# Kernel optimization log

Measured on AMD Instinct MI355X. Metric: run time of the kernel, lower is better.

The kernel has to match this reference:

```python
import jax, jax.numpy as jnp
import numpy as np
from jax import lax

H, MEM, AUX = 1024, 256, 16
S = MEM + AUX          # total_slots
B, T = 8, 4096
TOPK = 8               # top_k_binding
GAMMA, BETA, PTS = 0.92, 0.08, 0.4  # gamma, beta, prediction_torque_scale
RANK = 10              # coupling_rank == prediction_rank


def _inv_softplus(v):
    return float(np.log(np.expm1(max(float(v), 1e-6))))


def setup_inputs() -> dict:
    key = jax.random.key(0)
    ks = jax.random.split(key, 8)
    x = jax.random.normal(ks[0], (B, T, H), dtype=jnp.float32)
    # base basis: orthonormal columns in the first MEM slots (memory_dim < hidden_dim -> QR branch)
    q, _ = jnp.linalg.qr(jax.random.normal(ks[1], (H, MEM), dtype=jnp.float32))
    basis = jnp.zeros((H, S), jnp.float32).at[:, :MEM].set(q)
    return dict(
        x=x,
        basis=basis,
        tape_init_re=jax.random.normal(ks[2], (S,), dtype=jnp.float32) / S ** 0.5,
        tape_init_im=jax.random.normal(ks[3], (S,), dtype=jnp.float32) / S ** 0.5,
        eta_raw=jnp.asarray(_inv_softplus(0.08), jnp.float32),
        alpha=jnp.asarray(0.35, jnp.float32),
        torque_rotation=jnp.zeros((S,), jnp.float32),
        w_r=jnp.zeros((S,), jnp.float32),
        breadth_gate=jnp.zeros((S,), jnp.float32),
        epsilon_factor=jax.random.normal(ks[4], (S, RANK), dtype=jnp.float32) * 0.02,
        epsilon_scale=jnp.zeros((RANK,), jnp.float32),
        epsilon_diag=jnp.zeros((S,), jnp.float32),
        pred_factor=jax.random.normal(ks[5], (S, RANK), dtype=jnp.float32) * 0.02,
        pred_scale=jnp.zeros((RANK,), jnp.float32),
        pred_diag=jnp.zeros((S,), jnp.float32),
    )


def _forward(x, basis, tape_init_re, tape_init_im, eta_raw, alpha,
             torque_rotation, w_r, breadth_gate,
             epsilon_factor, epsilon_scale, epsilon_diag,
             pred_factor, pred_scale, pred_diag):
    active = jnp.arange(S) < MEM                      # base slots active (fixed population)
    amf = active.astype(jnp.float32)
    eta = jax.nn.softplus(eta_raw)
    # low-rank Hermitian coupling epsilon and prediction operator W_pred
    eps = (epsilon_factor * epsilon_scale) @ epsilon_factor.T + jnp.diag(epsilon_diag)
    wp = (pred_factor * pred_scale) @ pred_factor.T + jnp.diag(pred_diag)
    eps_c = eps.astype(jnp.complex64)
    wp_c = wp.astype(jnp.complex64)
    rot = jnp.exp(1j * torque_rotation.astype(jnp.complex64))  # torque phase rotation
    wr_gate = jax.nn.sigmoid(w_r)
    bg = jax.nn.sigmoid(breadth_gate)

    def renorm(tape):
        masked = tape * amf
        nrm = jnp.sqrt(jnp.maximum((jnp.abs(masked) ** 2).sum(-1, keepdims=True), 1e-16))
        return masked / nrm

    tape0 = (tape_init_re + 1j * tape_init_im) * amf   # aux slots zeroed as in _complex_tape_init
    tape0 = renorm(jnp.broadcast_to(tape0, (B, S)))

    def step(carry, x_t):
        tape, prev = carry                              # [B,S] complex64 each
        m = jnp.einsum('hs,bh->bs', basis, x_t)         # project into slot space
        mag = jnp.abs(m) * amf
        kth = lax.top_k(mag, TOPK)[0][:, -1:]           # top-k binding threshold
        inj = jnp.where((mag >= kth) & active, m, 0.0).astype(jnp.complex64)
        rotated = tape * rot
        drive = jnp.einsum('st,bt->bs', eps_c, rotated)  # coupling drive
        pred = jnp.einsum('st,bt->bs', wp_c, rotated)    # prediction torque
        new = (GAMMA * rotated + eta * drive + BETA * inj
               + PTS * 1j * pred + wr_gate * prev)
        new = renorm(new)
        y = x_t + alpha * jnp.einsum('hs,bs->bh', basis, bg * new.real)
        return (new, tape), y

    (_, _), ys = lax.scan(step, (tape0, tape0), jnp.swapaxes(x, 0, 1))
    return jnp.swapaxes(ys, 0, 1)


def reference(x, basis, tape_init_re, tape_init_im, eta_raw, alpha,
              torque_rotation, w_r, breadth_gate,
              epsilon_factor, epsilon_scale, epsilon_diag,
              pred_factor, pred_scale, pred_diag):
    return _forward(x, basis, tape_init_re, tape_init_im, eta_raw, alpha,
                    torque_rotation, w_r, breadth_gate,
                    epsilon_factor, epsilon_scale, epsilon_diag,
                    pred_factor, pred_scale, pred_diag)
```

## Files before the change

### kernel.cpp

```cpp
#include <hip/hip_runtime.h>
#include <cstdint>
#include <cstddef>

#define HD    1024
#define SLOTS 272
#define MEMS  256
#define BATCH 8
#define TT    4096
#define RR    (BATCH*TT)
#define RANKC 10

#define GAMMA 0.92f
#define BETA  0.08f
#define PTS   0.4f

typedef float f32x2 __attribute__((ext_vector_type(2)));
#define PKFMA(a, b, c) __builtin_elementwise_fma((a), (b), (c))

#define DPP_ADD(v, ctrl, rmask)                                                   \
    v += __int_as_float(__builtin_amdgcn_update_dpp(                              \
        0, __float_as_int(v), (ctrl), (rmask), 0xf, true))

__device__ __forceinline__ float wave_sum_bcast(float v)
{
    DPP_ADD(v, 0xB1,  0xf);
    DPP_ADD(v, 0x4E,  0xf);
    DPP_ADD(v, 0x141, 0xf);
    DPP_ADD(v, 0x140, 0xf);
    DPP_ADD(v, 0x142, 0xa);
    DPP_ADD(v, 0x143, 0xc);
    return __int_as_float(__builtin_amdgcn_readlane(__float_as_int(v), 63));
}

__global__ void prep_kernel(const float* __restrict__ t0re, const float* __restrict__ t0im,
                            const float* __restrict__ eta_raw,
                            const float* __restrict__ trot, const float* __restrict__ w_r,
                            const float* __restrict__ bgate,
                            const float* __restrict__ eps_scale, const float* __restrict__ pred_scale,
                            const float* __restrict__ eps_diag, const float* __restrict__ pred_diag,
                            float* __restrict__ consts, int* __restrict__ flags)
{
    __shared__ float red[MEMS];
    const int s = threadIdx.x;
    const float tr = t0re[s], ti = t0im[s];
    red[s] = tr * tr + ti * ti;
    __syncthreads();
    for (int off = 128; off > 0; off >>= 1) {
        if (s < off) red[s] += red[s + off];
        __syncthreads();
    }
    const float nrm = sqrtf(fmaxf(red[0], 1e-16f));
    const float eta = log1pf(expf(eta_raw[0]));
    const float rc = cosf(trot[s]), rs = sinf(trot[s]);
    const float c1 = GAMMA + eta * eps_diag[s];
    const float c2 = PTS * pred_diag[s];
    consts[0 * MEMS + s] = 1.0f / (1.0f + expf(-w_r[s]));
    consts[1 * MEMS + s] = 1.0f / (1.0f + expf(-bgate[s]));
    consts[2 * MEMS + s] = c1 * rc - c2 * rs;
    consts[3 * MEMS + s] = c1 * rs + c2 * rc;
    consts[4 * MEMS + s] = tr / nrm;
    consts[5 * MEMS + s] = ti / nrm;
    consts[6 * MEMS + s] = rc;
    consts[7 * MEMS + s] = rs;
    if (s == 0) {
        consts[8 * MEMS] = eta;
        int f1 = 0, f2 = 0;
        for (int k = 0; k < RANKC; ++k) {
            if (eps_scale[k]  != 0.0f) f1 = 1;
            if (pred_scale[k] != 0.0f) f2 = 1;
        }
        flags[0] = f1;
        flags[1] = f2;
    }
}

__global__ __launch_bounds__(256) void proj_topk_kernel(const float* __restrict__ x,
                                                        const float* __restrict__ basis,
                                                        float* __restrict__ M)
{
    __shared__ float pAs[16][64];
    __shared__ float pBs[16][260];
    const int tid  = threadIdx.x;
    const size_t row0 = (size_t)blockIdx.x * 64;
    const int mt = tid >> 5;
    const int nt = tid & 31;
    const int ar = tid >> 2;
    const int ak = (tid & 3) * 4;
    const int bk = tid >> 4;
    const int bn = (tid & 15) * 16;
    float acc[2][2][4][4] = {};
    for (int k0 = 0; k0 < HD; k0 += 16) {
        {
            const float4 av = *(const float4*)&x[(row0 + ar) * HD + k0 + ak];
            pAs[ak + 0][ar] = av.x; pAs[ak + 1][ar] = av.y;
            pAs[ak + 2][ar] = av.z; pAs[ak + 3][ar] = av.w;
#pragma unroll
            for (int c = 0; c < 4; ++c) {
                const float4 bv = *(const float4*)&basis[(size_t)(k0 + bk) * SLOTS + bn + c * 4];
                *(float4*)&pBs[bk][bn + c * 4] = bv;
            }
        }
        __syncthreads();
#pragma unroll
        for (int kk = 0; kk < 16; ++kk) {
            const float4 a0 = *(const float4*)&pAs[kk][mt * 4];
            const float4 a1 = *(const float4*)&pAs[kk][32 + mt * 4];
            const float4 b0 = *(const float4*)&pBs[kk][nt * 4];
            const float4 b1 = *(const float4*)&pBs[kk][128 + nt * 4];
            const float av[2][4] = {{a0.x, a0.y, a0.z, a0.w}, {a1.x, a1.y, a1.z, a1.w}};
            const float bv[2][4] = {{b0.x, b0.y, b0.z, b0.w}, {b1.x, b1.y, b1.z, b1.w}};
#pragma unroll
            for (int p = 0; p < 2; ++p)
#pragma unroll
                for (int q = 0; q < 2; ++q)
#pragma unroll
                    for (int i = 0; i < 4; ++i)
#pragma unroll
                        for (int j = 0; j < 4; ++j)
                            acc[p][q][i][j] += av[p][i] * bv[q][j];
        }
        __syncthreads();
    }
#pragma unroll
    for (int p = 0; p < 2; ++p)
#pragma unroll
        for (int i = 0; i < 4; ++i) {
            float v[8], a[8], w8[8];
#pragma unroll
            for (int q = 0; q < 2; ++q)
#pragma unroll
                for (int j = 0; j < 4; ++j) {
                    v[q * 4 + j] = acc[p][q][i][j];
                    a[q * 4 + j] = fabsf(v[q * 4 + j]);
                    w8[q * 4 + j] = a[q * 4 + j];
                }
            float kv = 0.0f;
#pragma unroll
            for (int it = 0; it < 8; ++it) {
                float lm = w8[0]; int li = 0;
#pragma unroll
                for (int e = 1; e < 8; ++e)
                    if (w8[e] > lm) { lm = w8[e]; li = e; }
                float bm = lm; int bi = nt * 8 + li;
#pragma unroll
                for (int off = 1; off < 32; off <<= 1) {
                    float om = __shfl_xor(bm, off);
                    int   oi = __shfl_xor(bi, off);
                    if (om > bm || (om == bm && oi < bi)) { bm = om; bi = oi; }
                }
                kv = bm;
                if ((bi >> 3) == nt) w8[bi & 7] = -1.0f;
            }
            const int r = p * 32 + mt * 4 + i;
#pragma unroll
            for (int q = 0; q < 2; ++q) {
                float4 o;
                o.x = (a[q * 4 + 0] >= kv) ? BETA * v[q * 4 + 0] : 0.0f;
                o.y = (a[q * 4 + 1] >= kv) ? BETA * v[q * 4 + 1] : 0.0f;
                o.z = (a[q * 4 + 2] >= kv) ? BETA * v[q * 4 + 2] : 0.0f;
                o.w = (a[q * 4 + 3] >= kv) ? BETA * v[q * 4 + 3] : 0.0f;
                *(float4*)&M[(row0 + r) * MEMS + q * 128 + nt * 4] = o;
            }
        }
}

__global__ __launch_bounds__(64) void scan_kernel(const float* __restrict__ M,
                                                  const float* __restrict__ consts,
                                                  const int* __restrict__ flags,
                                                  const float* __restrict__ eps_fac,
                                                  const float* __restrict__ eps_scale,
                                                  const float* __restrict__ eps_diag,
                                                  const float* __restrict__ pred_fac,
                                                  const float* __restrict__ pred_scale,
                                                  const float* __restrict__ pred_diag,
                                                  float* __restrict__ Wout)
{
    const int b    = blockIdx.x;
    const int lane = threadIdx.x;
    const int s0   = lane * 4;
    const int general = flags[0] | flags[1];
    const size_t base = (size_t)b * TT * MEMS + s0;

    if (!general) {
        f32x2 wrg[2], A2[2], B2[2];
        f32x2 wre[2], wim[2], qre[2], qim[2];
        {
            const float4 w4 = *(const float4*)&consts[0 * MEMS + s0];
            const float4 a4 = *(const float4*)&consts[2 * MEMS + s0];
            const float4 b4 = *(const float4*)&consts[3 * MEMS + s0];
            const float4 r4 = *(const float4*)&consts[4 * MEMS + s0];
            const float4 i4 = *(const float4*)&consts[5 * MEMS + s0];
            wrg[0] = {w4.x, w4.y};  wrg[1] = {w4.z, w4.w};
            A2[0]  = {a4.x, a4.y};  A2[1]  = {a4.z, a4.w};
            B2[0]  = {b4.x, b4.y};  B2[1]  = {b4.z, b4.w};
            wre[0] = {r4.x, r4.y};  wre[1] = {r4.z, r4.w};
            wim[0] = {i4.x, i4.y};  wim[1] = {i4.z, i4.w};
            qre[0] = wre[0]; qre[1] = wre[1];
            qim[0] = wim[0]; qim[1] = wim[1];
        }
        float ssp;
        {
            const f32x2 p0 = PKFMA(wim[0], wim[0], wre[0] * wre[0]);
            const f32x2 p1 = PKFMA(wim[1], wim[1], wre[1] * wre[1]);
            const f32x2 pp = p0 + p1;
            ssp = pp.x + pp.y;
        }
        float4 mbuf[16];
#pragma unroll
        for (int j = 0; j < 16; ++j)
            mbuf[j] = *(const float4*)&M[base + (size_t)j * MEMS];
        for (int t0 = 0; t0 < TT; t0 += 16) {
#pragma unroll
            for (int j = 0; j < 16; ++j) {
                const int t = t0 + j;
                const float4 mc = mbuf[j];
                mbuf[j] = *(const float4*)&M[base + (size_t)(t + 16) * MEMS];
                const float stot = wave_sum_bcast(ssp);
                const float icv  = __builtin_amdgcn_rsqf(fmaxf(stot, 1e-16f));
                const f32x2 ic2  = {icv, icv};
                const f32x2 Lr0 = PKFMA(A2[0], wre[0], -(B2[0] * wim[0]));
                const f32x2 Li0 = PKFMA(B2[0], wre[0],  A2[0] * wim[0]);
                const f32x2 Lr1 = PKFMA(A2[1], wre[1], -(B2[1] * wim[1]));
                const f32x2 Li1 = PKFMA(B2[1], wre[1],  A2[1] * wim[1]);
                const f32x2 m0 = {mc.x, mc.y};
                const f32x2 m1 = {mc.z, mc.w};
                const f32x2 Wr0 = PKFMA(wrg[0], qre[0], m0);
                const f32x2 Wi0 = wrg[0] * qim[0];
                const f32x2 Wr1 = PKFMA(wrg[1], qre[1], m1);
                const f32x2 Wi1 = wrg[1] * qim[1];
                const f32x2 u1r0 = PKFMA(ic2, Lr0, Wr0);
                const f32x2 u1i0 = PKFMA(ic2, Li0, Wi0);
                const f32x2 u1r1 = PKFMA(ic2, Lr1, Wr1);
                const f32x2 u1i1 = PKFMA(ic2, Li1, Wi1);
                const f32x2 ps0 = PKFMA(u1i0, u1i0, u1r0 * u1r0);
                const f32x2 ps1 = PKFMA(u1i1, u1i1, u1r1 * u1r1);
                const f32x2 pp  = ps0 + ps1;
                const f32x2 nr0 = wre[0] * ic2, ni0 = wim[0] * ic2;
                const f32x2 nr1 = wre[1] * ic2, ni1 = wim[1] * ic2;
                const int trow = t ? (t - 1) : 0;
                const float4 st4 = {nr0.x, nr0.y, nr1.x, nr1.y};
                *(float4*)&Wout[base + (size_t)trow * MEMS] = st4;
                qre[0] = nr0;  qim[0] = ni0;  qre[1] = nr1;  qim[1] = ni1;
                wre[0] = u1r0; wim[0] = u1i0; wre[1] = u1r1; wim[1] = u1i1;
                ssp = pp.x + pp.y;
            }
        }
        {
            const float stot = wave_sum_bcast(ssp);
            const float icv  = __builtin_amdgcn_rsqf(fmaxf(stot, 1e-16f));
            const float4 wq4 = {wre[0].x * icv, wre[0].y * icv,
                                wre[1].x * icv, wre[1].y * icv};
            *(float4*)&Wout[base + (size_t)(TT - 1) * MEMS] = wq4;
        }
        return;
    }

    float wr4[4], ur[4], ui[4], pr[4], pi[4];
    float rc4[4], rs4[4], ed4[4], pd4[4];
#pragma unroll
    for (int i = 0; i < 4; ++i) {
        wr4[i] = consts[0 * MEMS + s0 + i];
        ur[i]  = consts[4 * MEMS + s0 + i];
        ui[i]  = consts[5 * MEMS + s0 + i];
        pr[i] = ur[i]; pi[i] = ui[i];
        rc4[i] = consts[6 * MEMS + s0 + i];
        rs4[i] = consts[7 * MEMS + s0 + i];
        ed4[i] = eps_diag[s0 + i];
        pd4[i] = pred_diag[s0 + i];
    }
    const float eta  = consts[8 * MEMS];
    const int es_any = flags[0];
    const int ps_any = flags[1];
    float4 mbuf[4];
#pragma unroll
    for (int j = 0; j < 4; ++j)
        mbuf[j] = *(const float4*)&M[base + (size_t)j * MEMS];
    for (int t0 = 0; t0 < TT; t0 += 4) {
#pragma unroll
        for (int j = 0; j < 4; ++j) {
            const int t = t0 + j;
            const float4 mc = mbuf[j];
            const int pft = (t + 4 < TT) ? (t + 4) : (TT - 1);
            mbuf[j] = *(const float4*)&M[base + (size_t)pft * MEMS];
            float rr[4], ri[4], nr[4], ni[4];
#pragma unroll
            for (int i = 0; i < 4; ++i) {
                rr[i] = ur[i] * rc4[i] - ui[i] * rs4[i];
                ri[i] = ur[i] * rs4[i] + ui[i] * rc4[i];
            }
            const float mv[4] = {mc.x, mc.y, mc.z, mc.w};
#pragma unroll
            for (int i = 0; i < 4; ++i) {
                nr[i] = GAMMA * rr[i] + wr4[i] * pr[i] + eta * ed4[i] * rr[i]
                        - PTS * pd4[i] * ri[i] + mv[i];
                ni[i] = GAMMA * ri[i] + wr4[i] * pi[i] + eta * ed4[i] * ri[i]
                        + PTS * pd4[i] * rr[i];
            }
            if (es_any) {
#pragma unroll
                for (int k = 0; k < RANKC; ++k) {
                    float u[4], prj = 0.0f, pij = 0.0f;
#pragma unroll
                    for (int i = 0; i < 4; ++i) {
                        u[i] = eps_fac[(size_t)(s0 + i) * RANKC + k];
                        prj = fmaf(u[i], rr[i], prj);
                        pij = fmaf(u[i], ri[i], pij);
                    }
                    prj = wave_sum_bcast(prj);
                    pij = wave_sum_bcast(pij);
                    const float sc = eta * eps_scale[k];
#pragma unroll
                    for (int i = 0; i < 4; ++i) {
                        nr[i] = fmaf(sc * u[i], prj, nr[i]);
                        ni[i] = fmaf(sc * u[i], pij, ni[i]);
                    }
                }
            }
            if (ps_any) {
#pragma unroll
                for (int k = 0; k < RANKC; ++k) {
                    float u[4], qrj = 0.0f, qij = 0.0f;
#pragma unroll
                    for (int i = 0; i < 4; ++i) {
                        u[i] = pred_fac[(size_t)(s0 + i) * RANKC + k];
                        qrj = fmaf(u[i], rr[i], qrj);
                        qij = fmaf(u[i], ri[i], qij);
                    }
                    qrj = wave_sum_bcast(qrj);
                    qij = wave_sum_bcast(qij);
                    const float sc = PTS * pred_scale[k];
#pragma unroll
                    for (int i = 0; i < 4; ++i) {
                        nr[i] = fmaf(-sc * u[i], qij, nr[i]);
                        ni[i] = fmaf( sc * u[i], qrj, ni[i]);
                    }
                }
            }
            float ss = 0.0f;
#pragma unroll
            for (int i = 0; i < 4; ++i) ss = fmaf(nr[i], nr[i], fmaf(ni[i], ni[i], ss));
            ss = wave_sum_bcast(ss);
            const float inv = __builtin_amdgcn_rsqf(fmaxf(ss, 1e-16f));
#pragma unroll
            for (int i = 0; i < 4; ++i) {
                pr[i] = ur[i]; pi[i] = ui[i];
                ur[i] = nr[i] * inv; ui[i] = ni[i] * inv;
            }
            const float4 wq = {ur[0], ur[1], ur[2], ur[3]};
            *(float4*)&Wout[base + (size_t)t * MEMS] = wq;
        }
    }
}

__global__ __launch_bounds__(256) void outp_kernel(const float* __restrict__ W,
                                                   const float* __restrict__ basis,
                                                   const float* __restrict__ x,
                                                   const float* __restrict__ alpha_p,
                                                   const float* __restrict__ consts,
                                                   float* __restrict__ y)
{
    __shared__ float oAs[16][64];
    __shared__ float oBs[16][260];
    const int tid  = threadIdx.x;
    const size_t row0 = (size_t)blockIdx.x * 64;
    const int col0 = blockIdx.y * 256;
    const int mt = tid >> 5;
    const int nt = tid & 31;
    const int ar = tid >> 2;
    const int ak = (tid & 3) * 4;
    const float alpha = alpha_p[0];
    const float* bgc  = consts + MEMS;
    float acc[2][2][4][4] = {};
    for (int k0 = 0; k0 < MEMS; k0 += 16) {
        {
            const float4 av = *(const float4*)&W[(row0 + ar) * MEMS + k0 + ak];
            oAs[ak + 0][ar] = av.x; oAs[ak + 1][ar] = av.y;
            oAs[ak + 2][ar] = av.z; oAs[ak + 3][ar] = av.w;
#pragma unroll
            for (int c = 0; c < 4; ++c) {
                const float4 bv  = *(const float4*)&basis[(size_t)(col0 + tid) * SLOTS + k0 + c * 4];
                const float4 bg4 = *(const float4*)&bgc[k0 + c * 4];
                oBs[c * 4 + 0][tid] = bv.x * (alpha * bg4.x);
                oBs[c * 4 + 1][tid] = bv.y * (alpha * bg4.y);
                oBs[c * 4 + 2][tid] = bv.z * (alpha * bg4.z);
                oBs[c * 4 + 3][tid] = bv.w * (alpha * bg4.w);
            }
        }
        __syncthreads();
#pragma unroll
        for (int kk = 0; kk < 16; ++kk) {
            const float4 a0 = *(const float4*)&oAs[kk][mt * 4];
            const float4 a1 = *(const float4*)&oAs[kk][32 + mt * 4];
            const float4 b0 = *(const float4*)&oBs[kk][nt * 4];
            const float4 b1 = *(const float4*)&oBs[kk][128 + nt * 4];
            const float av[2][4] = {{a0.x, a0.y, a0.z, a0.w}, {a1.x, a1.y, a1.z, a1.w}};
            const float bv[2][4] = {{b0.x, b0.y, b0.z, b0.w}, {b1.x, b1.y, b1.z, b1.w}};
#pragma unroll
            for (int p = 0; p < 2; ++p)
#pragma unroll
                for (int q = 0; q < 2; ++q)
#pragma unroll
                    for (int i = 0; i < 4; ++i)
#pragma unroll
                        for (int j = 0; j < 4; ++j)
                            acc[p][q][i][j] += av[p][i] * bv[q][j];
        }
        __syncthreads();
    }
#pragma unroll
    for (int p = 0; p < 2; ++p)
#pragma unroll
        for (int i = 0; i < 4; ++i) {
            const size_t r = row0 + p * 32 + mt * 4 + i;
#pragma unroll
            for (int q = 0; q < 2; ++q) {
                const size_t ro = r * HD + col0 + q * 128 + nt * 4;
                const float4 xv = *(const float4*)&x[ro];
                const float4 o  = {xv.x + acc[p][q][i][0], xv.y + acc[p][q][i][1],
                                   xv.z + acc[p][q][i][2], xv.w + acc[p][q][i][3]};
                *(float4*)&y[ro] = o;
            }
        }
}

extern "C" void kernel_launch(void* const* d_in, const int* in_sizes, int n_in,
                              void* d_out, int out_size, void* d_ws, size_t ws_size,
                              hipStream_t stream)
{
    const float* x          = (const float*)d_in[0];
    const float* basis      = (const float*)d_in[1];
    const float* t0re       = (const float*)d_in[2];
    const float* t0im       = (const float*)d_in[3];
    const float* eta_raw    = (const float*)d_in[4];
    const float* alpha      = (const float*)d_in[5];
    const float* trot       = (const float*)d_in[6];
    const float* w_r        = (const float*)d_in[7];
    const float* bgate      = (const float*)d_in[8];
    const float* eps_fac    = (const float*)d_in[9];
    const float* eps_scale  = (const float*)d_in[10];
    const float* eps_diag   = (const float*)d_in[11];
    const float* pred_fac   = (const float*)d_in[12];
    const float* pred_scale = (const float*)d_in[13];
    const float* pred_diag  = (const float*)d_in[14];
    float* out = (float*)d_out;

    const size_t szM = (size_t)RR * MEMS * sizeof(float);
    const size_t szW = szM;
    const size_t szC = 16384;

    char* ws = (char*)d_ws;
    float *Mbuf, *Wbuf, *cbuf;
    if (ws_size >= szM + szW + szC) {
        Mbuf = (float*)(ws);
        Wbuf = (float*)(ws + szM);
        cbuf = (float*)(ws + szM + szW);
    } else {
        Mbuf = (float*)d_out;
        Wbuf = (float*)(ws);
        cbuf = (float*)(ws + szW);
    }
    int* fbuf = (int*)(cbuf + 8 * MEMS + 16);

    prep_kernel<<<1, 256, 0, stream>>>(t0re, t0im, eta_raw, trot, w_r, bgate,
                                       eps_scale, pred_scale, eps_diag, pred_diag,
                                       cbuf, fbuf);
    proj_topk_kernel<<<RR / 64, 256, 0, stream>>>(x, basis, Mbuf);
    scan_kernel<<<BATCH, 64, 0, stream>>>(Mbuf, cbuf, fbuf,
                                          eps_fac, eps_scale, eps_diag,
                                          pred_fac, pred_scale, pred_diag,
                                          Wbuf);
    outp_kernel<<<dim3(RR / 64, HD / 256), 256, 0, stream>>>(Wbuf, basis, x, alpha,
                                                             cbuf, out);
}
```

Baseline: 1.040 ms.

## Compute output projection with bf16 MFMA and a prescaled bf16 basis

Replaces the fp32 LDS-tiled FMA GEMM in the output projection with bf16 MFMA 16x16x32 instructions. A new small kernel prescales the basis by alpha and the breadth gate and stores it as bf16. The scan output W is converted to bf16 in registers and fed straight to MFMA without shared memory. This lowers the compute cost of the GEMM but reduces precision and writes y with scalar stores instead of float4, which may lose coalescing.

New measurement: 991.5 us. 1.05x faster.

```diff
diff --git a/kernel.cpp b/kernel.cpp
--- a/kernel.cpp
+++ b/kernel.cpp
@@ -15,6 +15,8 @@
 #define PTS   0.4f
 
 typedef float f32x2 __attribute__((ext_vector_type(2)));
+typedef float f32x4 __attribute__((ext_vector_type(4)));
+typedef short bf16x8 __attribute__((ext_vector_type(8)));
 #define PKFMA(a, b, c) __builtin_elementwise_fma((a), (b), (c))
 
 #define DPP_ADD(v, ctrl, rmask)                                                   \
@@ -30,6 +32,13 @@
     DPP_ADD(v, 0x142, 0xa);
     DPP_ADD(v, 0x143, 0xc);
     return __int_as_float(__builtin_amdgcn_readlane(__float_as_int(v), 63));
+}
+
+__device__ __forceinline__ unsigned short f2bf(float f)
+{
+    unsigned u = __float_as_uint(f);
+    u = (u + 0x7FFFu + ((u >> 16) & 1u)) >> 16;
+    return (unsigned short)u;
 }
 
 __global__ void prep_kernel(const float* __restrict__ t0re, const float* __restrict__ t0im,
@@ -72,6 +81,17 @@
         flags[0] = f1;
         flags[1] = f2;
     }
+}
+
+__global__ void gprep_kernel(const float* __restrict__ basis,
+                             const float* __restrict__ alpha_p,
+                             const float* __restrict__ consts,
+                             unsigned short* __restrict__ G)
+{
+    const int h = blockIdx.x;
+    const int k = threadIdx.x;
+    const float g = alpha_p[0] * consts[MEMS + k] * basis[(size_t)h * SLOTS + k];
+    G[(size_t)h * MEMS + k] = f2bf(g);
 }
 
 __global__ __launch_bounds__(256) void proj_topk_kernel(const float* __restrict__ x,
@@ -353,74 +373,50 @@
 }
 
 __global__ __launch_bounds__(256) void outp_kernel(const float* __restrict__ W,
-                                                   const float* __restrict__ basis,
+                                                   const unsigned short* __restrict__ G,
                                                    const float* __restrict__ x,
-                                                   const float* __restrict__ alpha_p,
-                                                   const float* __restrict__ consts,
                                                    float* __restrict__ y)
 {
-    __shared__ float oAs[16][64];
-    __shared__ float oBs[16][260];
-    const int tid  = threadIdx.x;
-    const size_t row0 = (size_t)blockIdx.x * 64;
+    const int tid = threadIdx.x;
+    const int w   = tid >> 6;
+    const int l   = tid & 63;
+    const int ln  = l & 15;
+    const int lk  = (l >> 4) * 8;
+    const size_t row0 = (size_t)blockIdx.x * 64 + (size_t)w * 16;
     const int col0 = blockIdx.y * 256;
-    const int mt = tid >> 5;
-    const int nt = tid & 31;
-    const int ar = tid >> 2;
-    const int ak = (tid & 3) * 4;
-    const float alpha = alpha_p[0];
-    const float* bgc  = consts + MEMS;
-    float acc[2][2][4][4] = {};
-    for (int k0 = 0; k0 < MEMS; k0 += 16) {
-        {
-            const float4 av = *(const float4*)&W[(row0 + ar) * MEMS + k0 + ak];
-            oAs[ak + 0][ar] = av.x; oAs[ak + 1][ar] = av.y;
-            oAs[ak + 2][ar] = av.z; oAs[ak + 3][ar] = av.w;
-#pragma unroll
-            for (int c = 0; c < 4; ++c) {
-                const float4 bv  = *(const float4*)&basis[(size_t)(col0 + tid) * SLOTS + k0 + c * 4];
-                const float4 bg4 = *(const float4*)&bgc[k0 + c * 4];
-                oBs[c * 4 + 0][tid] = bv.x * (alpha * bg4.x);
-                oBs[c * 4 + 1][tid] = bv.y * (alpha * bg4.y);
-                oBs[c * 4 + 2][tid] = bv.z * (alpha * bg4.z);
-                oBs[c * 4 + 3][tid] = bv.w * (alpha * bg4.w);
-            }
-        }
-        __syncthreads();
-#pragma unroll
-        for (int kk = 0; kk < 16; ++kk) {
-            const float4 a0 = *(const float4*)&oAs[kk][mt * 4];
-            const float4 a1 = *(const float4*)&oAs[kk][32 + mt * 4];
-            const float4 b0 = *(const float4*)&oBs[kk][nt * 4];
-            const float4 b1 = *(const float4*)&oBs[kk][128 + nt * 4];
-            const float av[2][4] = {{a0.x, a0.y, a0.z, a0.w}, {a1.x, a1.y, a1.z, a1.w}};
-            const float bv[2][4] = {{b0.x, b0.y, b0.z, b0.w}, {b1.x, b1.y, b1.z, b1.w}};
-#pragma unroll
-            for (int p = 0; p < 2; ++p)
-#pragma unroll
-                for (int q = 0; q < 2; ++q)
-#pragma unroll
-                    for (int i = 0; i < 4; ++i)
-#pragma unroll
-                        for (int j = 0; j < 4; ++j)
-                            acc[p][q][i][j] += av[p][i] * bv[q][j];
-        }
-        __syncthreads();
-    }
-#pragma unroll
-    for (int p = 0; p < 2; ++p)
+
+    bf16x8 af[8];
+    {
+        const float* wrow = &W[(row0 + ln) * MEMS];
+#pragma unroll
+        for (int c = 0; c < 8; ++c) {
+            const float4 a0 = *(const float4*)&wrow[c * 32 + lk];
+            const float4 a1 = *(const float4*)&wrow[c * 32 + lk + 4];
+            bf16x8 f;
+            f[0] = (short)f2bf(a0.x); f[1] = (short)f2bf(a0.y);
+            f[2] = (short)f2bf(a0.z); f[3] = (short)f2bf(a0.w);
+            f[4] = (short)f2bf(a1.x); f[5] = (short)f2bf(a1.y);
+            f[6] = (short)f2bf(a1.z); f[7] = (short)f2bf(a1.w);
+            af[c] = f;
+        }
+    }
+#pragma unroll
+    for (int ct = 0; ct < 16; ++ct) {
+        const int h = col0 + ct * 16 + ln;
+        const unsigned short* grow = &G[(size_t)h * MEMS + lk];
+        f32x4 acc = {0.0f, 0.0f, 0.0f, 0.0f};
+#pragma unroll
+        for (int c = 0; c < 8; ++c) {
+            const bf16x8 bf = *(const bf16x8*)&grow[c * 32];
+            acc = __builtin_amdgcn_mfma_f32_16x16x32_bf16(af[c], bf, acc, 0, 0, 0);
+        }
+        const size_t rbase = (row0 + (size_t)((l >> 4) * 4)) * HD + h;
 #pragma unroll
         for (int i = 0; i < 4; ++i) {
-            const size_t r = row0 + p * 32 + mt * 4 + i;
-#pragma unroll
-            for (int q = 0; q < 2; ++q) {
-                const size_t ro = r * HD + col0 + q * 128 + nt * 4;
-                const float4 xv = *(const float4*)&x[ro];
-                const float4 o  = {xv.x + acc[p][q][i][0], xv.y + acc[p][q][i][1],
-                                   xv.z + acc[p][q][i][2], xv.w + acc[p][q][i][3]};
-                *(float4*)&y[ro] = o;
-            }
-        }
+            const size_t ro = rbase + (size_t)i * HD;
+            y[ro] = x[ro] + acc[i];
+        }
+    }
 }
 
 extern "C" void kernel_launch(void* const* d_in, const int* in_sizes, int n_in,
@@ -447,28 +443,32 @@
     const size_t szM = (size_t)RR * MEMS * sizeof(float);
     const size_t szW = szM;
     const size_t szC = 16384;
+    const size_t szG = (size_t)HD * MEMS * 2;
 
     char* ws = (char*)d_ws;
     float *Mbuf, *Wbuf, *cbuf;
-    if (ws_size >= szM + szW + szC) {
+    unsigned short* Gbuf;
+    if (ws_size >= szM + szW + szC + szG) {
         Mbuf = (float*)(ws);
         Wbuf = (float*)(ws + szM);
         cbuf = (float*)(ws + szM + szW);
+        Gbuf = (unsigned short*)(ws + szM + szW + szC);
     } else {
         Mbuf = (float*)d_out;
         Wbuf = (float*)(ws);
         cbuf = (float*)(ws + szW);
+        Gbuf = (unsigned short*)(ws + szW + szC);
     }
     int* fbuf = (int*)(cbuf + 8 * MEMS + 16);
 
     prep_kernel<<<1, 256, 0, stream>>>(t0re, t0im, eta_raw, trot, w_r, bgate,
                                        eps_scale, pred_scale, eps_diag, pred_diag,
                                        cbuf, fbuf);
+    gprep_kernel<<<HD, 256, 0, stream>>>(basis, alpha, cbuf, Gbuf);
     proj_topk_kernel<<<RR / 64, 256, 0, stream>>>(x, basis, Mbuf);
     scan_kernel<<<BATCH, 64, 0, stream>>>(Mbuf, cbuf, fbuf,
                                           eps_fac, eps_scale, eps_diag,
                                           pred_fac, pred_scale, pred_diag,
                                           Wbuf);
-    outp_kernel<<<dim3(RR / 64, HD / 256), 256, 0, stream>>>(Wbuf, basis, x, alpha,
-                                                             cbuf, out);
-}
+    outp_kernel<<<dim3(RR / 64, HD / 256), 256, 0, stream>>>(Wbuf, Gbuf, x, out);
+}
```
